# Kernel optimization log

Measured on AMD Instinct MI355X. Metric: run time of the kernel, lower is better.

## Reference

```python
import jax, jax.numpy as jnp
import numpy as np

E = 8        # num_experts
K = 2        # num_experts_per_tok
H = 1024     # hidden_dim
F = 2816     # intermediate_dim
R = 256      # shared-core rank
B, S = 2, 1024


def setup_inputs() -> dict:
    key = jax.random.key(0)
    ks = jax.random.split(key, 12)
    inp = {
        "hidden_states": jax.random.normal(ks[0], (B, S, H), jnp.float32),
        "gate_w": jax.random.normal(ks[1], (H, E), jnp.float32) / np.sqrt(H),
        # gate_proj: hidden -> intermediate, factored W_e = Ug[e] @ Cg @ Vg[e]
        "Ug": jax.random.normal(ks[2], (E, H, R), jnp.float32) / np.sqrt(H),
        "Cg": jax.random.normal(ks[3], (R, R), jnp.float32) / np.sqrt(R),
        "Vg": jax.random.normal(ks[4], (E, R, F), jnp.float32) / np.sqrt(R),
        # up_proj: hidden -> intermediate
        "Uu": jax.random.normal(ks[5], (E, H, R), jnp.float32) / np.sqrt(H),
        "Cu": jax.random.normal(ks[6], (R, R), jnp.float32) / np.sqrt(R),
        "Vu": jax.random.normal(ks[7], (E, R, F), jnp.float32) / np.sqrt(R),
        # down_proj: intermediate -> hidden
        "Ud": jax.random.normal(ks[8], (E, F, R), jnp.float32) / np.sqrt(F),
        "Cd": jax.random.normal(ks[9], (R, R), jnp.float32) / np.sqrt(R),
        "Vd": jax.random.normal(ks[10], (E, R, H), jnp.float32) / np.sqrt(R),
    }
    return inp


def _moe_forward(x, gate_w, Ug, Cg, Vg, Uu, Cu, Vu, Ud, Cd, Vd):
    b, s, h = x.shape
    xf = x.reshape(-1, h)                       # [T, H]
    T = xf.shape[0]
    logits = xf @ gate_w                        # [T, E]
    probs = jax.nn.softmax(logits, axis=-1)
    w, idx = jax.lax.top_k(probs, K)            # [T, K]
    w = w / jnp.sum(w, axis=-1, keepdims=True)
    # dense combine weights: combine[t, e] = sum of renormalized routing
    # weights over top-k slots routed to expert e (scatter-add in torch code)
    combine = jnp.zeros((T, E), xf.dtype).at[jnp.arange(T)[:, None], idx].add(w)
    out = jnp.zeros_like(xf)
    for e in range(E):  # fixed small expert count
        g = (xf @ Ug[e]) @ Cg @ Vg[e]           # [T, F]
        u = (xf @ Uu[e]) @ Cu @ Vu[e]           # [T, F]
        a = jax.nn.silu(g) * u
        y = (a @ Ud[e]) @ Cd @ Vd[e]            # [T, H]
        out = out + combine[:, e:e + 1] * y
    return out.reshape(b, s, h)


def reference(hidden_states, gate_w, Ug, Cg, Vg, Uu, Cu, Vu, Ud, Cd, Vd):
    return _moe_forward(hidden_states, gate_w, Ug, Cg, Vg, Uu, Cu, Vu, Ud, Cd, Vd)
```

## Files before the change

### kernel.cpp

```cpp
#include <hip/hip_runtime.h>
#include <math.h>

constexpr int cE = 8;
constexpr int cH = 1024;
constexpr int cF = 2816;
constexpr int cR = 256;
constexpr int cT = 2048;
constexpr int ROWS = cT * 2;
constexpr int LDA = 40;

using short8  = __attribute__((ext_vector_type(8))) short;
using float4v = __attribute__((ext_vector_type(4))) float;
#define MFMA16 __builtin_amdgcn_mfma_f32_16x16x32_bf16

__device__ __forceinline__ unsigned short f2bf(float f) {
  union { float f; unsigned u; } v; v.f = f;
  unsigned r = v.u + 0x7fffu + ((v.u >> 16) & 1u);
  return (unsigned short)(r >> 16);
}
__device__ __forceinline__ float bf2f(unsigned short s) {
  union { unsigned u; float f; } v; v.u = (unsigned)s << 16; return v.f;
}

__device__ __forceinline__ void store_bf8(unsigned short* dst, float4 a, float4 b) {
  union { unsigned short u[8]; uint4 v; } t;
  t.u[0] = f2bf(a.x); t.u[1] = f2bf(a.y); t.u[2] = f2bf(a.z); t.u[3] = f2bf(a.w);
  t.u[4] = f2bf(b.x); t.u[5] = f2bf(b.y); t.u[6] = f2bf(b.z); t.u[7] = f2bf(b.w);
  *reinterpret_cast<uint4*>(dst) = t.v;
}

__device__ __forceinline__ void gld16(const unsigned short* g, unsigned short* l) {
  __builtin_amdgcn_global_load_lds(
      (const __attribute__((address_space(1))) void*)g,
      (__attribute__((address_space(3))) void*)l, 16, 0, 0);
}

constexpr int TCONV_BLOCKS = 19072;
constexpr int PREP1_BLOCKS = TCONV_BLOCKS + cT / 4;

__device__ __forceinline__ void tconv_tile(
    const float* __restrict__ in, unsigned short* __restrict__ out,
    int P, int Q, int e, int bx, int by, int tid, float (*tile)[33])
{
  const long es = (long)P * Q;
  in += e * es; out += e * es;
  const int c0 = bx * 32, r0 = by * 32;
  const int r = tid >> 3, c4 = (tid & 7) * 4;
  float4 v = *reinterpret_cast<const float4*>(in + (long)(r0 + r) * Q + c0 + c4);
  tile[r][c4 + 0] = v.x; tile[r][c4 + 1] = v.y;
  tile[r][c4 + 2] = v.z; tile[r][c4 + 3] = v.w;
  __syncthreads();
  const int cc = tid >> 3, rr4 = (tid & 7) * 4;
  ushort4 o;
  o.x = f2bf(tile[rr4 + 0][cc]);
  o.y = f2bf(tile[rr4 + 1][cc]);
  o.z = f2bf(tile[rr4 + 2][cc]);
  o.w = f2bf(tile[rr4 + 3][cc]);
  *reinterpret_cast<ushort4*>(out + (long)(c0 + cc) * P + r0 + rr4) = o;
}

__global__ __launch_bounds__(256) void k_prep1(
    const float* __restrict__ Cg, unsigned short* __restrict__ CgT,
    const float* __restrict__ Cu, unsigned short* __restrict__ CuT,
    const float* __restrict__ Vd, unsigned short* __restrict__ VdT,
    const float* __restrict__ Vg, unsigned short* __restrict__ vgT,
    const float* __restrict__ Vu, unsigned short* __restrict__ vuT,
    const float* __restrict__ Ud, unsigned short* __restrict__ udT,
    const float* __restrict__ x, const float* __restrict__ gw,
    unsigned short* __restrict__ xb, int* __restrict__ et,
    float* __restrict__ wt)
{
  __shared__ float tile[32][33];
  int b = blockIdx.x;
  const int tid = threadIdx.x;
  if (b < TCONV_BLOCKS) {
    const float* in; unsigned short* out; int P, Q;
    if (b < 64)         { in = Cg; out = CgT; P = 256;  Q = 256;  }
    else if (b < 128)   { b -= 64;    in = Cu; out = CuT; P = 256;  Q = 256;  }
    else if (b < 2176)  { b -= 128;   in = Vd; out = VdT; P = 256;  Q = 1024; }
    else if (b < 7808)  { b -= 2176;  in = Vg; out = vgT; P = 256;  Q = 2816; }
    else if (b < 13440) { b -= 7808;  in = Vu; out = vuT; P = 256;  Q = 2816; }
    else                { b -= 13440; in = Ud; out = udT; P = 2816; Q = 256;  }
    const int tpe = (P / 32) * (Q / 32);
    const int e = b / tpe, rem = b % tpe;
    const int bx = rem % (Q / 32), by = rem / (Q / 32);
    tconv_tile(in, out, P, Q, e, bx, by, tid, tile);
    return;
  }
  const int wid = tid >> 6, lane = tid & 63;
  const int t = (b - TCONV_BLOCKS) * 4 + wid;
  const float* xr = x + (long)t * cH + lane * 16;
  float4 v0 = *reinterpret_cast<const float4*>(xr);
  float4 v1 = *reinterpret_cast<const float4*>(xr + 4);
  float4 v2 = *reinterpret_cast<const float4*>(xr + 8);
  float4 v3 = *reinterpret_cast<const float4*>(xr + 12);
  store_bf8(xb + (long)t * cH + lane * 16, v0, v1);
  store_bf8(xb + (long)t * cH + lane * 16 + 8, v2, v3);
  float xv[16];
  *reinterpret_cast<float4*>(&xv[0])  = v0;
  *reinterpret_cast<float4*>(&xv[4])  = v1;
  *reinterpret_cast<float4*>(&xv[8])  = v2;
  *reinterpret_cast<float4*>(&xv[12]) = v3;
  const float* g = gw + (long)lane * 16 * cE;
  float l[cE];
#pragma unroll
  for (int e = 0; e < cE; ++e) l[e] = 0.f;
#pragma unroll
  for (int i = 0; i < 16; ++i) {
    float4 ga = *reinterpret_cast<const float4*>(g + i * cE);
    float4 gb = *reinterpret_cast<const float4*>(g + i * cE + 4);
    float xi = xv[i];
    l[0] += xi * ga.x; l[1] += xi * ga.y; l[2] += xi * ga.z; l[3] += xi * ga.w;
    l[4] += xi * gb.x; l[5] += xi * gb.y; l[6] += xi * gb.z; l[7] += xi * gb.w;
  }
#pragma unroll
  for (int m = 1; m < 64; m <<= 1)
#pragma unroll
    for (int e = 0; e < cE; ++e)
      l[e] += __shfl_xor(l[e], m, 64);
  if (lane == 0) {
    int i0 = 0; float m0 = l[0];
#pragma unroll
    for (int e = 1; e < cE; ++e) if (l[e] > m0) { m0 = l[e]; i0 = e; }
    int i1 = -1; float m1 = -1e30f;
#pragma unroll
    for (int e = 0; e < cE; ++e) if (e != i0 && l[e] > m1) { m1 = l[e]; i1 = e; }
    float w0 = 1.f / (1.f + expf(m1 - m0));
    et[t * 2 + 0] = i0;  et[t * 2 + 1] = i1;
    wt[t * 2 + 0] = w0;  wt[t * 2 + 1] = 1.f - w0;
  }
}

__device__ __forceinline__ void foldm_body(
    const unsigned short* __restrict__ A, const float* __restrict__ B,
    unsigned short* __restrict__ D, int ldd, int m0, int n0, int tid,
    unsigned short* As, unsigned short* Bs)
{
  const int sr = tid >> 2, sk = (tid & 3) * 8;
  const unsigned short* a0 = A + (long)(m0 + sr) * 256 + sk;
  const unsigned short* a1 = a0 + (long)64 * 256;
  const float* br = B + (long)(n0 + sr) * 256 + sk;
  uint4 rA0, rA1; float4 rB0, rB1;
  auto load_slice = [&](int k0) {
    rA0 = *reinterpret_cast<const uint4*>(a0 + k0);
    rA1 = *reinterpret_cast<const uint4*>(a1 + k0);
    rB0 = *reinterpret_cast<const float4*>(br + k0);
    rB1 = *reinterpret_cast<const float4*>(br + k0 + 4);
  };
  load_slice(0);
  const int wid = tid >> 6, lane = tid & 63;
  const int wm = (wid >> 1) * 64, wn = (wid & 1) * 32;
  const int fr = lane & 15, fq = lane >> 4;
  float4v zf = {0.f, 0.f, 0.f, 0.f};
  float4v acc[4][2];
#pragma unroll
  for (int i = 0; i < 4; ++i) { acc[i][0] = zf; acc[i][1] = zf; }
  for (int k0 = 0; k0 < 256; k0 += 32) {
    *reinterpret_cast<uint4*>(&As[sr * LDA + sk]) = rA0;
    *reinterpret_cast<uint4*>(&As[(sr + 64) * LDA + sk]) = rA1;
    store_bf8(&Bs[sr * LDA + sk], rB0, rB1);
    if (k0 + 32 < 256) load_slice(k0 + 32);
    __syncthreads();
    short8 af[4], bf[2];
#pragma unroll
    for (int mi = 0; mi < 4; ++mi)
      af[mi] = *reinterpret_cast<const short8*>(&As[(wm + mi * 16 + fr) * LDA + fq * 8]);
#pragma unroll
    for (int nj = 0; nj < 2; ++nj)
      bf[nj] = *reinterpret_cast<const short8*>(&Bs[(wn + nj * 16 + fr) * LDA + fq * 8]);
#pragma unroll
    for (int mi = 0; mi < 4; ++mi)
#pragma unroll
      for (int nj = 0; nj < 2; ++nj)
        acc[mi][nj] = MFMA16(af[mi], bf[nj], acc[mi][nj], 0, 0, 0);
    __syncthreads();
  }
#pragma unroll
  for (int mi = 0; mi < 4; ++mi)
#pragma unroll
    for (int r = 0; r < 4; ++r) {
      int m = m0 + wm + mi * 16 + fq * 4 + r;
#pragma unroll
      for (int nj = 0; nj < 2; ++nj)
        D[(long)m * ldd + n0 + wn + nj * 16 + fr] = f2bf(acc[mi][nj][r]);
    }
}

constexpr int PREP2_BLOCKS = 512 + 256 + 1;
__global__ __launch_bounds__(256, 2) void k_prep2(
    const unsigned short* __restrict__ CgT, const unsigned short* __restrict__ CuT,
    const float* __restrict__ Ug, const float* __restrict__ Uu,
    unsigned short* __restrict__ b1t,
    const unsigned short* __restrict__ VdT, const float* __restrict__ Cd,
    unsigned short* __restrict__ vd2t,
    const int* __restrict__ et, int* __restrict__ rowmap,
    int* __restrict__ tok, int* __restrict__ cnt, int* __restrict__ off)
{
  __shared__ __align__(16) unsigned short As[128 * LDA], Bs[64 * LDA];
  __shared__ int sc_[cE], sp_[cE], so_[cE];
  const int b = blockIdx.x;
  const int tid = threadIdx.x;
  if (b < 512) {
    const int bx = b & 15, by = (b >> 4) & 1, z = b >> 5;
    const int sel = z >> 3, e = z & 7;
    const unsigned short* A = sel ? CuT : CgT;
    const float* B = (sel ? Uu : Ug) + (long)e * cH * cR;
    unsigned short* Dp = b1t + (long)e * 512 * 1024 + (long)sel * 256 * 1024;
    foldm_body(A, B, Dp, cH, by * 128, bx * 64, tid, As, Bs);
  } else if (b < 768) {
    const int b2 = b - 512;
    const int bx = b2 & 3, by = (b2 >> 2) & 7, e = b2 >> 5;
    foldm_body(VdT + (long)e * cH * cR, Cd, vd2t + (long)e * cH * 256, cR,
               by * 128, bx * 64, tid, As, Bs);
  } else {
    if (tid < cE) { sc_[tid] = 0; sp_[tid] = 0; }
    __syncthreads();
    for (int i = tid; i < ROWS; i += 256) atomicAdd(&sc_[et[i]], 1);
    __syncthreads();
    if (tid == 0) {
      int s = 0;
      for (int e = 0; e < cE; ++e) { so_[e] = s; s += sc_[e]; }
    }
    __syncthreads();
    for (int i = tid; i < ROWS; i += 256) {
      int e = et[i];
      int slot = atomicAdd(&sp_[e], 1);
      int cr = so_[e] + slot;
      rowmap[i] = cr;
      tok[cr] = i >> 1;
    }
    if (tid < cE) { cnt[tid] = sc_[tid]; off[tid] = so_[tid]; }
  }
}

__global__ __launch_bounds__(256, 2) void k_t1c(
    const unsigned short* __restrict__ xb, const unsigned short* __restrict__ b1t,
    unsigned short* __restrict__ t1, const int* __restrict__ tok,
    const int* __restrict__ cnt, const int* __restrict__ off)
{
  __shared__ __align__(16) unsigned short As[128 * 64], Bs[64 * 64];
  const int e = blockIdx.z, c = cnt[e], o = off[e];
  const int m0 = blockIdx.y * 128;
  if (m0 >= c) return;
  const int n0 = blockIdx.x * 64;
  const int tid = threadIdx.x;
  const int wid = tid >> 6, lane = tid & 63;
  const int sr8 = lane >> 3, sc = (lane & 7) * 8;
  const unsigned short* gA[4];
#pragma unroll
  for (int j = 0; j < 4; ++j) {
    int row = min(m0 + wid * 32 + j * 8 + sr8, c - 1);
    gA[j] = xb + (long)tok[o + row] * cH + sc;
  }
  const unsigned short* gB = b1t + (long)e * 512 * 1024 +
      (long)(n0 + wid * 16 + sr8) * 1024 + sc;
  unsigned short* lA = As + wid * 32 * 64;
  unsigned short* lB = Bs + wid * 16 * 64;
  const int wm = (wid >> 1) * 64, wn = (wid & 1) * 32;
  const int fr = lane & 15, fq = lane >> 4;
  float4v zf = {0.f, 0.f, 0.f, 0.f};
  float4v acc[4][2];
#pragma unroll
  for (int i = 0; i < 4; ++i) { acc[i][0] = zf; acc[i][1] = zf; }
  for (int k0 = 0; k0 < cH; k0 += 64) {
#pragma unroll
    for (int j = 0; j < 4; ++j) gld16(gA[j] + k0, lA + j * 8 * 64);
    gld16(gB + k0, lB);
    gld16(gB + (long)8 * 1024 + k0, lB + 8 * 64);
    __syncthreads();
#pragma unroll
    for (int ks = 0; ks < 2; ++ks) {
      short8 af[4], bf[2];
#pragma unroll
      for (int mi = 0; mi < 4; ++mi)
        af[mi] = *reinterpret_cast<const short8*>(
            &As[(wm + mi * 16 + fr) * 64 + ks * 32 + fq * 8]);
#pragma unroll
      for (int nj = 0; nj < 2; ++nj)
        bf[nj] = *reinterpret_cast<const short8*>(
            &Bs[(wn + nj * 16 + fr) * 64 + ks * 32 + fq * 8]);
#pragma unroll
      for (int mi = 0; mi < 4; ++mi)
#pragma unroll
        for (int nj = 0; nj < 2; ++nj)
          acc[mi][nj] = MFMA16(af[mi], bf[nj], acc[mi][nj], 0, 0, 0);
    }
    __syncthreads();
  }
#pragma unroll
  for (int mi = 0; mi < 4; ++mi)
#pragma unroll
    for (int r = 0; r < 4; ++r) {
      int row = m0 + wm + mi * 16 + fq * 4 + r;
      if (row < c) {
#pragma unroll
        for (int nj = 0; nj < 2; ++nj)
          t1[(long)(o + row) * 512 + n0 + wn + nj * 16 + fr] = f2bf(acc[mi][nj][r]);
      }
    }
}

__global__ __launch_bounds__(256, 2) void k_act(
    const unsigned short* __restrict__ t1,
    const unsigned short* __restrict__ vgT, const unsigned short* __restrict__ vuT,
    unsigned short* __restrict__ a, const int* __restrict__ cnt,
    const int* __restrict__ off)
{
  __shared__ __align__(16) unsigned short Ag[128 * 32], Au[128 * 32];
  __shared__ __align__(16) unsigned short Bg[64 * 32],  Bu[64 * 32];
  const int e = blockIdx.z, c = cnt[e], o = off[e];
  const int m0 = blockIdx.y * 128;
  if (m0 >= c) return;
  const int n0 = blockIdx.x * 64;
  const int tid = threadIdx.x;
  const int wid = tid >> 6, lane = tid & 63;
  const int sr16 = lane >> 2, sc = (lane & 3) * 8;
  const int ra0 = o + min(m0 + wid * 32 + sr16, c - 1);
  const int ra1 = o + min(m0 + wid * 32 + 16 + sr16, c - 1);
  const unsigned short* gAg0 = t1 + (long)ra0 * 512 + sc;
  const unsigned short* gAg1 = t1 + (long)ra1 * 512 + sc;
  const unsigned short* gBg = vgT + (long)e * cF * 256 + (long)(n0 + wid * 16 + sr16) * 256 + sc;
  const unsigned short* gBu = vuT + (long)e * cF * 256 + (long)(n0 + wid * 16 + sr16) * 256 + sc;
  unsigned short* lAg = Ag + wid * 32 * 32;
  unsigned short* lAu = Au + wid * 32 * 32;
  unsigned short* lBg = Bg + wid * 16 * 32;
  unsigned short* lBu = Bu + wid * 16 * 32;
  const int wm = (wid >> 1) * 64, wn = (wid & 1) * 32;
  const int fr = lane & 15, fq = lane >> 4;
  float4v zf = {0.f, 0.f, 0.f, 0.f};
  float4v accg[4][2], accu[4][2];
#pragma unroll
  for (int i = 0; i < 4; ++i) { accg[i][0] = zf; accg[i][1] = zf; accu[i][0] = zf; accu[i][1] = zf; }
  for (int k0 = 0; k0 < 256; k0 += 32) {
    gld16(gAg0 + k0, lAg);
    gld16(gAg1 + k0, lAg + 16 * 32);
    gld16(gAg0 + 256 + k0, lAu);
    gld16(gAg1 + 256 + k0, lAu + 16 * 32);
    gld16(gBg + k0, lBg);
    gld16(gBu + k0, lBu);
    __syncthreads();
    short8 ag[4], au[4], bg[2], bu[2];
#pragma unroll
    for (int mi = 0; mi < 4; ++mi) {
      ag[mi] = *reinterpret_cast<const short8*>(&Ag[(wm + mi * 16 + fr) * 32 + fq * 8]);
      au[mi] = *reinterpret_cast<const short8*>(&Au[(wm + mi * 16 + fr) * 32 + fq * 8]);
    }
#pragma unroll
    for (int nj = 0; nj < 2; ++nj) {
      bg[nj] = *reinterpret_cast<const short8*>(&Bg[(wn + nj * 16 + fr) * 32 + fq * 8]);
      bu[nj] = *reinterpret_cast<const short8*>(&Bu[(wn + nj * 16 + fr) * 32 + fq * 8]);
    }
#pragma unroll
    for (int mi = 0; mi < 4; ++mi)
#pragma unroll
      for (int nj = 0; nj < 2; ++nj) {
        accg[mi][nj] = MFMA16(ag[mi], bg[nj], accg[mi][nj], 0, 0, 0);
        accu[mi][nj] = MFMA16(au[mi], bu[nj], accu[mi][nj], 0, 0, 0);
      }
    __syncthreads();
  }
#pragma unroll
  for (int mi = 0; mi < 4; ++mi)
#pragma unroll
    for (int r = 0; r < 4; ++r) {
      int row = m0 + wm + mi * 16 + fq * 4 + r;
      if (row < c) {
#pragma unroll
        for (int nj = 0; nj < 2; ++nj) {
          float g = accg[mi][nj][r];
          float u = accu[mi][nj][r];
          float s = g / (1.f + expf(-g)) * u;
          a[(long)(o + row) * cF + n0 + wn + nj * 16 + fr] = f2bf(s);
        }
      }
    }
}

__global__ __launch_bounds__(256, 2) void k_t3(
    const unsigned short* __restrict__ a, const unsigned short* __restrict__ udT,
    unsigned short* __restrict__ t3b, const int* __restrict__ cnt,
    const int* __restrict__ off)
{
  __shared__ __align__(16) unsigned short As[64 * 64], Bs[64 * 64];
  const int e = blockIdx.z, c = cnt[e], o = off[e];
  const int m0 = blockIdx.y * 64;
  if (m0 >= c) return;
  const int n0 = blockIdx.x * 64;
  const int tid = threadIdx.x;
  const int wid = tid >> 6, lane = tid & 63;
  const int sr8 = lane >> 3, sc = (lane & 7) * 8;
  const int ra0 = o + min(m0 + wid * 16 + sr8, c - 1);
  const int ra1 = o + min(m0 + wid * 16 + 8 + sr8, c - 1);
  const unsigned short* gA0 = a + (long)ra0 * cF + sc;
  const unsigned short* gA1 = a + (long)ra1 * cF + sc;
  const unsigned short* gB  = udT + (long)e * 256 * cF + (long)(n0 + wid * 16 + sr8) * cF + sc;
  unsigned short* lA = As + wid * 16 * 64;
  unsigned short* lB = Bs + wid * 16 * 64;
  const int wm = (wid >> 1) * 32, wn = (wid & 1) * 32;
  const int fr = lane & 15, fq = lane >> 4;
  float4v zf = {0.f, 0.f, 0.f, 0.f};
  float4v acc[2][2] = {{zf, zf}, {zf, zf}};
  for (int k0 = 0; k0 < cF; k0 += 64) {
    gld16(gA0 + k0, lA);
    gld16(gA1 + k0, lA + 8 * 64);
    gld16(gB + k0, lB);
    gld16(gB + (long)8 * cF + k0, lB + 8 * 64);
    __syncthreads();
#pragma unroll
    for (int ks = 0; ks < 2; ++ks) {
      short8 af[2], bf[2];
#pragma unroll
      for (int mi = 0; mi < 2; ++mi)
        af[mi] = *reinterpret_cast<const short8*>(
            &As[(wm + mi * 16 + fr) * 64 + ks * 32 + fq * 8]);
#pragma unroll
      for (int nj = 0; nj < 2; ++nj)
        bf[nj] = *reinterpret_cast<const short8*>(
            &Bs[(wn + nj * 16 + fr) * 64 + ks * 32 + fq * 8]);
#pragma unroll
      for (int mi = 0; mi < 2; ++mi)
#pragma unroll
        for (int nj = 0; nj < 2; ++nj)
          acc[mi][nj] = MFMA16(af[mi], bf[nj], acc[mi][nj], 0, 0, 0);
    }
    __syncthreads();
  }
#pragma unroll
  for (int mi = 0; mi < 2; ++mi)
#pragma unroll
    for (int r = 0; r < 4; ++r) {
      int row = m0 + wm + mi * 16 + fq * 4 + r;
      if (row < c) {
        unsigned short* dst = t3b + (long)(o + row) * 256 + n0 + wn;
#pragma unroll
        for (int nj = 0; nj < 2; ++nj)
          dst[nj * 16 + fr] = f2bf(acc[mi][nj][r]);
      }
    }
}

__global__ __launch_bounds__(256, 2) void k_y(
    const unsigned short* __restrict__ t3b, const unsigned short* __restrict__ vd2t,
    unsigned short* __restrict__ y, const int* __restrict__ cnt,
    const int* __restrict__ off)
{
  __shared__ __align__(16) unsigned short As[128 * 32], Bs[64 * 32];
  const int e = blockIdx.z, c = cnt[e], o = off[e];
  const int m0 = blockIdx.y * 128;
  if (m0 >= c) return;
  const int n0 = blockIdx.x * 64;
  const int tid = threadIdx.x;
  const int wid = tid >> 6, lane = tid & 63;
  const int sr16 = lane >> 2, sc = (lane & 3) * 8;
  const int ra0 = o + min(m0 + wid * 32 + sr16, c - 1);
  const int ra1 = o + min(m0 + wid * 32 + 16 + sr16, c - 1);
  const unsigned short* gA0 = t3b + (long)ra0 * 256 + sc;
  const unsigned short* gA1 = t3b + (long)ra1 * 256 + sc;
  const unsigned short* gB  = vd2t + (long)e * cH * 256 + (long)(n0 + wid * 16 + sr16) * 256 + sc;
  unsigned short* lA = As + wid * 32 * 32;
  unsigned short* lB = Bs + wid * 16 * 32;
  const int wm = (wid >> 1) * 64, wn = (wid & 1) * 32;
  const int fr = lane & 15, fq = lane >> 4;
  float4v zf = {0.f, 0.f, 0.f, 0.f};
  float4v acc[4][2];
#pragma unroll
  for (int i = 0; i < 4; ++i) { acc[i][0] = zf; acc[i][1] = zf; }
  for (int k0 = 0; k0 < 256; k0 += 32) {
    gld16(gA0 + k0, lA);
    gld16(gA1 + k0, lA + 16 * 32);
    gld16(gB + k0, lB);
    __syncthreads();
    short8 af[4], bf[2];
#pragma unroll
    for (int mi = 0; mi < 4; ++mi)
      af[mi] = *reinterpret_cast<const short8*>(&As[(wm + mi * 16 + fr) * 32 + fq * 8]);
#pragma unroll
    for (int nj = 0; nj < 2; ++nj)
      bf[nj] = *reinterpret_cast<const short8*>(&Bs[(wn + nj * 16 + fr) * 32 + fq * 8]);
#pragma unroll
    for (int mi = 0; mi < 4; ++mi)
#pragma unroll
      for (int nj = 0; nj < 2; ++nj)
        acc[mi][nj] = MFMA16(af[mi], bf[nj], acc[mi][nj], 0, 0, 0);
    __syncthreads();
  }
#pragma unroll
  for (int mi = 0; mi < 4; ++mi)
#pragma unroll
    for (int r = 0; r < 4; ++r) {
      int row = m0 + wm + mi * 16 + fq * 4 + r;
      if (row < c) {
#pragma unroll
        for (int nj = 0; nj < 2; ++nj)
          y[(long)(o + row) * cH + n0 + wn + nj * 16 + fr] = f2bf(acc[mi][nj][r]);
      }
    }
}

__global__ __launch_bounds__(256) void k_combine(
    const unsigned short* __restrict__ y, const float* __restrict__ wt,
    const int* __restrict__ rowmap, float* __restrict__ out)
{
  const int tid = threadIdx.x;
  const int t = blockIdx.x * 2 + (tid >> 7);
  const int h = (tid & 127) * 8;
  const int r0 = rowmap[2 * t], r1 = rowmap[2 * t + 1];
  const float w0 = wt[2 * t], w1 = wt[2 * t + 1];
  union { uint4 v; unsigned short s[8]; } ua, ub;
  ua.v = *reinterpret_cast<const uint4*>(y + (long)r0 * cH + h);
  ub.v = *reinterpret_cast<const uint4*>(y + (long)r1 * cH + h);
  float o[8];
#pragma unroll
  for (int i = 0; i < 8; ++i)
    o[i] = w0 * bf2f(ua.s[i]) + w1 * bf2f(ub.s[i]);
  float* dst = out + (long)t * cH + h;
  *reinterpret_cast<float4*>(dst)     = make_float4(o[0], o[1], o[2], o[3]);
  *reinterpret_cast<float4*>(dst + 4) = make_float4(o[4], o[5], o[6], o[7]);
}

extern "C" void kernel_launch(void* const* d_in, const int* in_sizes, int n_in,
                              void* d_out, int out_size, void* d_ws, size_t ws_size,
                              hipStream_t stream)
{
  const float* x  = (const float*)d_in[0];
  const float* gw = (const float*)d_in[1];
  const float* Ug = (const float*)d_in[2];
  const float* Cg = (const float*)d_in[3];
  const float* Vg = (const float*)d_in[4];
  const float* Uu = (const float*)d_in[5];
  const float* Cu = (const float*)d_in[6];
  const float* Vu = (const float*)d_in[7];
  const float* Ud = (const float*)d_in[8];
  const float* Cd = (const float*)d_in[9];
  const float* Vd = (const float*)d_in[10];
  float* out = (float*)d_out;

  char* w = (char*)d_ws;
  unsigned short* vgT = (unsigned short*)w;
  unsigned short* t3b = (unsigned short*)w;
  w += (long)cE * cF * 256 * 2;
  unsigned short* b1t = (unsigned short*)w;  w += (long)cE * 512 * 1024 * 2;
  unsigned short* vd2t = (unsigned short*)w; w += (long)cE * cH * 256 * 2;
  unsigned short* vuT = (unsigned short*)w;
  unsigned short* yb  = (unsigned short*)w;  w += (long)cE * cF * 256 * 2;
  unsigned short* udT = (unsigned short*)w;  w += (long)cE * 256 * cF * 2;
  unsigned short* VdT = (unsigned short*)w;  w += (long)cE * cH * 256 * 2;
  unsigned short* xb  = (unsigned short*)w;  w += (long)cT * cH * 2;
  unsigned short* CgT = (unsigned short*)w;  w += (long)cR * cR * 2;
  unsigned short* CuT = (unsigned short*)w;  w += (long)cR * cR * 2;
  unsigned short* t1  = (unsigned short*)w;  w += (long)ROWS * 512 * 2;
  unsigned short* ab  = (unsigned short*)w;  w += (long)ROWS * cF * 2;
  float* wt   = (float*)w; w += ROWS * 4;
  int* et     = (int*)w; w += ROWS * 4;
  int* rowmap = (int*)w; w += ROWS * 4;
  int* tok    = (int*)w; w += ROWS * 4;
  int* cnt = (int*)w; w += cE * 4;
  int* off = (int*)w; w += cE * 4;

  k_prep1<<<dim3(PREP1_BLOCKS), dim3(256), 0, stream>>>(
      Cg, CgT, Cu, CuT, Vd, VdT, Vg, vgT, Vu, vuT, Ud, udT, x, gw, xb, et, wt);
  k_prep2<<<dim3(PREP2_BLOCKS), dim3(256), 0, stream>>>(
      CgT, CuT, Ug, Uu, b1t, VdT, Cd, vd2t, et, rowmap, tok, cnt, off);
  k_t1c<<<dim3(8, cT / 128, cE), dim3(256), 0, stream>>>(xb, b1t, t1, tok, cnt, off);
  k_act<<<dim3(cF / 64, cT / 128, cE), dim3(256), 0, stream>>>(t1, vgT, vuT, ab, cnt, off);
  k_t3<<<dim3(4, cT / 64, cE), dim3(256), 0, stream>>>(ab, udT, t3b, cnt, off);
  k_y<<<dim3(cH / 64, cT / 128, cE), dim3(256), 0, stream>>>(t3b, vd2t, yb, cnt, off);
  k_combine<<<dim3(cT / 2), dim3(256), 0, stream>>>(yb, wt, rowmap, out);
}
```

Measured before the change: 308.1 us.

## Split-K the down-projection, widen transpose tiles, and deepen act K-step

```diff
diff --git a/kernel.cpp b/kernel.cpp
--- a/kernel.cpp
+++ b/kernel.cpp
@@ -35,29 +35,36 @@
       (__attribute__((address_space(3))) void*)l, 16, 0, 0);
 }
 
-constexpr int TCONV_BLOCKS = 19072;
-constexpr int PREP1_BLOCKS = TCONV_BLOCKS + cT / 4;
-
-__device__ __forceinline__ void tconv_tile(
+__device__ __forceinline__ void tconv_tile64(
     const float* __restrict__ in, unsigned short* __restrict__ out,
-    int P, int Q, int e, int bx, int by, int tid, float (*tile)[33])
+    int P, int Q, int e, int bx, int by, int tid, float (*tile)[65])
 {
   const long es = (long)P * Q;
   in += e * es; out += e * es;
-  const int c0 = bx * 32, r0 = by * 32;
-  const int r = tid >> 3, c4 = (tid & 7) * 4;
-  float4 v = *reinterpret_cast<const float4*>(in + (long)(r0 + r) * Q + c0 + c4);
-  tile[r][c4 + 0] = v.x; tile[r][c4 + 1] = v.y;
-  tile[r][c4 + 2] = v.z; tile[r][c4 + 3] = v.w;
+  const int c0 = bx * 64, r0 = by * 64;
+  const int r = tid >> 4, c4 = (tid & 15) * 4;
+#pragma unroll
+  for (int p = 0; p < 4; ++p) {
+    float4 v = *reinterpret_cast<const float4*>(
+        in + (long)(r0 + p * 16 + r) * Q + c0 + c4);
+    tile[p * 16 + r][c4 + 0] = v.x; tile[p * 16 + r][c4 + 1] = v.y;
+    tile[p * 16 + r][c4 + 2] = v.z; tile[p * 16 + r][c4 + 3] = v.w;
+  }
   __syncthreads();
-  const int cc = tid >> 3, rr4 = (tid & 7) * 4;
-  ushort4 o;
-  o.x = f2bf(tile[rr4 + 0][cc]);
-  o.y = f2bf(tile[rr4 + 1][cc]);
-  o.z = f2bf(tile[rr4 + 2][cc]);
-  o.w = f2bf(tile[rr4 + 3][cc]);
-  *reinterpret_cast<ushort4*>(out + (long)(c0 + cc) * P + r0 + rr4) = o;
-}
+  const int cc = tid >> 4, rr4 = (tid & 15) * 4;
+#pragma unroll
+  for (int p = 0; p < 4; ++p) {
+    ushort4 o;
+    o.x = f2bf(tile[rr4 + 0][p * 16 + cc]);
+    o.y = f2bf(tile[rr4 + 1][p * 16 + cc]);
+    o.z = f2bf(tile[rr4 + 2][p * 16 + cc]);
+    o.w = f2bf(tile[rr4 + 3][p * 16 + cc]);
+    *reinterpret_cast<ushort4*>(out + (long)(c0 + p * 16 + cc) * P + r0 + rr4) = o;
+  }
+}
+
+constexpr int TCONV_BLOCKS = 4768;
+constexpr int PREP1_BLOCKS = TCONV_BLOCKS + cT / 4;
 
 __global__ __launch_bounds__(256) void k_prep1(
     const float* __restrict__ Cg, unsigned short* __restrict__ CgT,
@@ -70,21 +77,21 @@
     unsigned short* __restrict__ xb, int* __restrict__ et,
     float* __restrict__ wt)
 {
-  __shared__ float tile[32][33];
+  __shared__ float tile[64][65];
   int b = blockIdx.x;
   const int tid = threadIdx.x;
   if (b < TCONV_BLOCKS) {
     const float* in; unsigned short* out; int P, Q;
-    if (b < 64)         { in = Cg; out = CgT; P = 256;  Q = 256;  }
-    else if (b < 128)   { b -= 64;    in = Cu; out = CuT; P = 256;  Q = 256;  }
-    else if (b < 2176)  { b -= 128;   in = Vd; out = VdT; P = 256;  Q = 1024; }
-    else if (b < 7808)  { b -= 2176;  in = Vg; out = vgT; P = 256;  Q = 2816; }
-    else if (b < 13440) { b -= 7808;  in = Vu; out = vuT; P = 256;  Q = 2816; }
-    else                { b -= 13440; in = Ud; out = udT; P = 2816; Q = 256;  }
-    const int tpe = (P / 32) * (Q / 32);
+    if (b < 16)         { in = Cg; out = CgT; P = 256;  Q = 256;  }
+    else if (b < 32)    { b -= 16;    in = Cu; out = CuT; P = 256;  Q = 256;  }
+    else if (b < 544)   { b -= 32;    in = Vd; out = VdT; P = 256;  Q = 1024; }
+    else if (b < 1952)  { b -= 544;   in = Vg; out = vgT; P = 256;  Q = 2816; }
+    else if (b < 3360)  { b -= 1952;  in = Vu; out = vuT; P = 256;  Q = 2816; }
+    else                { b -= 3360;  in = Ud; out = udT; P = 2816; Q = 256;  }
+    const int tpe = (P / 64) * (Q / 64);
     const int e = b / tpe, rem = b % tpe;
-    const int bx = rem % (Q / 32), by = rem / (Q / 32);
-    tconv_tile(in, out, P, Q, e, bx, by, tid, tile);
+    const int bx = rem % (Q / 64), by = rem / (Q / 64);
+    tconv_tile64(in, out, P, Q, e, bx, by, tid, tile);
     return;
   }
   const int wid = tid >> 6, lane = tid & 63;
@@ -306,57 +313,71 @@
     unsigned short* __restrict__ a, const int* __restrict__ cnt,
     const int* __restrict__ off)
 {
-  __shared__ __align__(16) unsigned short Ag[128 * 32], Au[128 * 32];
-  __shared__ __align__(16) unsigned short Bg[64 * 32],  Bu[64 * 32];
+  __shared__ __align__(16) unsigned short Ag[128 * 64], Au[128 * 64];
+  __shared__ __align__(16) unsigned short Bg[64 * 64],  Bu[64 * 64];
   const int e = blockIdx.z, c = cnt[e], o = off[e];
   const int m0 = blockIdx.y * 128;
   if (m0 >= c) return;
   const int n0 = blockIdx.x * 64;
   const int tid = threadIdx.x;
   const int wid = tid >> 6, lane = tid & 63;
-  const int sr16 = lane >> 2, sc = (lane & 3) * 8;
-  const int ra0 = o + min(m0 + wid * 32 + sr16, c - 1);
-  const int ra1 = o + min(m0 + wid * 32 + 16 + sr16, c - 1);
-  const unsigned short* gAg0 = t1 + (long)ra0 * 512 + sc;
-  const unsigned short* gAg1 = t1 + (long)ra1 * 512 + sc;
-  const unsigned short* gBg = vgT + (long)e * cF * 256 + (long)(n0 + wid * 16 + sr16) * 256 + sc;
-  const unsigned short* gBu = vuT + (long)e * cF * 256 + (long)(n0 + wid * 16 + sr16) * 256 + sc;
-  unsigned short* lAg = Ag + wid * 32 * 32;
-  unsigned short* lAu = Au + wid * 32 * 32;
-  unsigned short* lBg = Bg + wid * 16 * 32;
-  unsigned short* lBu = Bu + wid * 16 * 32;
+  const int sr8 = lane >> 3, sc8 = (lane & 7) * 8;
+  const unsigned short* gA[4];
+#pragma unroll
+  for (int j = 0; j < 4; ++j) {
+    int row = o + min(m0 + wid * 32 + j * 8 + sr8, c - 1);
+    gA[j] = t1 + (long)row * 512 + sc8;
+  }
+  const unsigned short* gBg = vgT + (long)e * cF * 256 +
+      (long)(n0 + wid * 16 + sr8) * 256 + sc8;
+  const unsigned short* gBu = vuT + (long)e * cF * 256 +
+      (long)(n0 + wid * 16 + sr8) * 256 + sc8;
+  unsigned short* lAg = Ag + wid * 32 * 64;
+  unsigned short* lAu = Au + wid * 32 * 64;
+  unsigned short* lBg = Bg + wid * 16 * 64;
+  unsigned short* lBu = Bu + wid * 16 * 64;
   const int wm = (wid >> 1) * 64, wn = (wid & 1) * 32;
   const int fr = lane & 15, fq = lane >> 4;
   float4v zf = {0.f, 0.f, 0.f, 0.f};
   float4v accg[4][2], accu[4][2];
 #pragma unroll
   for (int i = 0; i < 4; ++i) { accg[i][0] = zf; accg[i][1] = zf; accu[i][0] = zf; accu[i][1] = zf; }
-  for (int k0 = 0; k0 < 256; k0 += 32) {
-    gld16(gAg0 + k0, lAg);
-    gld16(gAg1 + k0, lAg + 16 * 32);
-    gld16(gAg0 + 256 + k0, lAu);
-    gld16(gAg1 + 256 + k0, lAu + 16 * 32);
-    gld16(gBg + k0, lBg);
-    gld16(gBu + k0, lBu);
-    __syncthreads();
-    short8 ag[4], au[4], bg[2], bu[2];
-#pragma unroll
-    for (int mi = 0; mi < 4; ++mi) {
-      ag[mi] = *reinterpret_cast<const short8*>(&Ag[(wm + mi * 16 + fr) * 32 + fq * 8]);
-      au[mi] = *reinterpret_cast<const short8*>(&Au[(wm + mi * 16 + fr) * 32 + fq * 8]);
-    }
-#pragma unroll
-    for (int nj = 0; nj < 2; ++nj) {
-      bg[nj] = *reinterpret_cast<const short8*>(&Bg[(wn + nj * 16 + fr) * 32 + fq * 8]);
-      bu[nj] = *reinterpret_cast<const short8*>(&Bu[(wn + nj * 16 + fr) * 32 + fq * 8]);
-    }
-#pragma unroll
-    for (int mi = 0; mi < 4; ++mi)
+  for (int k0 = 0; k0 < 256; k0 += 64) {
+#pragma unroll
+    for (int j = 0; j < 4; ++j) gld16(gA[j] + k0,       lAg + j * 8 * 64);
+#pragma unroll
+    for (int j = 0; j < 4; ++j) gld16(gA[j] + 256 + k0, lAu + j * 8 * 64);
+#pragma unroll
+    for (int j = 0; j < 2; ++j) {
+      gld16(gBg + (long)j * 8 * 256 + k0, lBg + j * 8 * 64);
+      gld16(gBu + (long)j * 8 * 256 + k0, lBu + j * 8 * 64);
+    }
+    __syncthreads();
+#pragma unroll
+    for (int ks = 0; ks < 2; ++ks) {
+      short8 ag[4], au[4], bg[2], bu[2];
+#pragma unroll
+      for (int mi = 0; mi < 4; ++mi) {
+        ag[mi] = *reinterpret_cast<const short8*>(
+            &Ag[(wm + mi * 16 + fr) * 64 + ks * 32 + fq * 8]);
+        au[mi] = *reinterpret_cast<const short8*>(
+            &Au[(wm + mi * 16 + fr) * 64 + ks * 32 + fq * 8]);
+      }
 #pragma unroll
       for (int nj = 0; nj < 2; ++nj) {
-        accg[mi][nj] = MFMA16(ag[mi], bg[nj], accg[mi][nj], 0, 0, 0);
-        accu[mi][nj] = MFMA16(au[mi], bu[nj], accu[mi][nj], 0, 0, 0);
+        bg[nj] = *reinterpret_cast<const short8*>(
+            &Bg[(wn + nj * 16 + fr) * 64 + ks * 32 + fq * 8]);
+        bu[nj] = *reinterpret_cast<const short8*>(
+            &Bu[(wn + nj * 16 + fr) * 64 + ks * 32 + fq * 8]);
       }
+#pragma unroll
+      for (int mi = 0; mi < 4; ++mi)
+#pragma unroll
+        for (int nj = 0; nj < 2; ++nj) {
+          accg[mi][nj] = MFMA16(ag[mi], bg[nj], accg[mi][nj], 0, 0, 0);
+          accu[mi][nj] = MFMA16(au[mi], bu[nj], accu[mi][nj], 0, 0, 0);
+        }
+    }
     __syncthreads();
   }
 #pragma unroll
@@ -378,29 +399,31 @@
 
 __global__ __launch_bounds__(256, 2) void k_t3(
     const unsigned short* __restrict__ a, const unsigned short* __restrict__ udT,
-    unsigned short* __restrict__ t3b, const int* __restrict__ cnt,
+    float* __restrict__ t3p, const int* __restrict__ cnt,
     const int* __restrict__ off)
 {
   __shared__ __align__(16) unsigned short As[64 * 64], Bs[64 * 64];
   const int e = blockIdx.z, c = cnt[e], o = off[e];
   const int m0 = blockIdx.y * 64;
   if (m0 >= c) return;
-  const int n0 = blockIdx.x * 64;
+  const int n0 = (blockIdx.x & 3) * 64;
+  const int ksp = blockIdx.x >> 2;
+  const int kbase = ksp * 1408;
   const int tid = threadIdx.x;
   const int wid = tid >> 6, lane = tid & 63;
   const int sr8 = lane >> 3, sc = (lane & 7) * 8;
   const int ra0 = o + min(m0 + wid * 16 + sr8, c - 1);
   const int ra1 = o + min(m0 + wid * 16 + 8 + sr8, c - 1);
-  const unsigned short* gA0 = a + (long)ra0 * cF + sc;
-  const unsigned short* gA1 = a + (long)ra1 * cF + sc;
-  const unsigned short* gB  = udT + (long)e * 256 * cF + (long)(n0 + wid * 16 + sr8) * cF + sc;
+  const unsigned short* gA0 = a + (long)ra0 * cF + kbase + sc;
+  const unsigned short* gA1 = a + (long)ra1 * cF + kbase + sc;
+  const unsigned short* gB  = udT + (long)e * 256 * cF + (long)(n0 + wid * 16 + sr8) * cF + kbase + sc;
   unsigned short* lA = As + wid * 16 * 64;
   unsigned short* lB = Bs + wid * 16 * 64;
   const int wm = (wid >> 1) * 32, wn = (wid & 1) * 32;
   const int fr = lane & 15, fq = lane >> 4;
   float4v zf = {0.f, 0.f, 0.f, 0.f};
   float4v acc[2][2] = {{zf, zf}, {zf, zf}};
-  for (int k0 = 0; k0 < cF; k0 += 64) {
+  for (int k0 = 0; k0 < 1408; k0 += 64) {
     gld16(gA0 + k0, lA);
     gld16(gA1 + k0, lA + 8 * 64);
     gld16(gB + k0, lB);
@@ -425,18 +448,33 @@
     }
     __syncthreads();
   }
+  float* dstbase = t3p + (long)ksp * ROWS * 256;
 #pragma unroll
   for (int mi = 0; mi < 2; ++mi)
 #pragma unroll
     for (int r = 0; r < 4; ++r) {
       int row = m0 + wm + mi * 16 + fq * 4 + r;
       if (row < c) {
-        unsigned short* dst = t3b + (long)(o + row) * 256 + n0 + wn;
+        float* dst = dstbase + (long)(o + row) * 256 + n0 + wn;
 #pragma unroll
         for (int nj = 0; nj < 2; ++nj)
-          dst[nj * 16 + fr] = f2bf(acc[mi][nj][r]);
+          dst[nj * 16 + fr] = acc[mi][nj][r];
       }
     }
+}
+
+__global__ __launch_bounds__(256) void k_red2(
+    const float* __restrict__ t3p, unsigned short* __restrict__ t3b)
+{
+  const long psz = (long)ROWS * 256;
+  long i = ((long)blockIdx.x * 256 + threadIdx.x) * 8;
+  float4 s0 = *reinterpret_cast<const float4*>(t3p + i);
+  float4 s1 = *reinterpret_cast<const float4*>(t3p + i + 4);
+  float4 a0 = *reinterpret_cast<const float4*>(t3p + psz + i);
+  float4 a1 = *reinterpret_cast<const float4*>(t3p + psz + i + 4);
+  s0.x += a0.x; s0.y += a0.y; s0.z += a0.z; s0.w += a0.w;
+  s1.x += a1.x; s1.y += a1.y; s1.z += a1.z; s1.w += a1.w;
+  store_bf8(t3b + i, s0, s1);
 }
 
 __global__ __launch_bounds__(256, 2) void k_y(
@@ -537,7 +575,8 @@
 
   char* w = (char*)d_ws;
   unsigned short* vgT = (unsigned short*)w;
-  unsigned short* t3b = (unsigned short*)w;
+  float*          t3p = (float*)w;
+  unsigned short* t3b = (unsigned short*)(w + (long)2 * ROWS * 256 * 4);
   w += (long)cE * cF * 256 * 2;
   unsigned short* b1t = (unsigned short*)w;  w += (long)cE * 512 * 1024 * 2;
   unsigned short* vd2t = (unsigned short*)w; w += (long)cE * cH * 256 * 2;
@@ -563,7 +602,8 @@
       CgT, CuT, Ug, Uu, b1t, VdT, Cd, vd2t, et, rowmap, tok, cnt, off);
   k_t1c<<<dim3(8, cT / 128, cE), dim3(256), 0, stream>>>(xb, b1t, t1, tok, cnt, off);
   k_act<<<dim3(cF / 64, cT / 128, cE), dim3(256), 0, stream>>>(t1, vgT, vuT, ab, cnt, off);
-  k_t3<<<dim3(4, cT / 64, cE), dim3(256), 0, stream>>>(ab, udT, t3b, cnt, off);
+  k_t3<<<dim3(8, cT / 64, cE), dim3(256), 0, stream>>>(ab, udT, t3p, cnt, off);
+  k_red2<<<dim3(ROWS * 256 / (256 * 8)), dim3(256), 0, stream>>>(t3p, t3b);
   k_y<<<dim3(cH / 64, cT / 128, cE), dim3(256), 0, stream>>>(t3b, vd2t, yb, cnt, off);
   k_combine<<<dim3(cT / 2), dim3(256), 0, stream>>>(yb, wt, rowmap, out);
 }
```

Result: no change. 304.8 us (-1.1%).
